# Optimization experiments

Hardware: AMD Instinct MI355X
Metric: run time of the kernel (lower is better)

## Reference

```python
import jax, jax.numpy as jnp
import numpy as np

D = 256  # input_dim
B = 2048

def setup_inputs() -> dict:
    key = jax.random.key(0)
    ks = jax.random.split(key, 6)
    x = jax.random.normal(ks[0], (B, D), dtype=jnp.float32)
    offsets = jax.random.normal(ks[1], (D,), dtype=jnp.float32)
    coeff0 = jax.random.normal(ks[2], (), dtype=jnp.float32)
    coeff1 = jax.random.normal(ks[3], (D,), dtype=jnp.float32)
    coeff2 = jax.random.normal(ks[4], (D, D), dtype=jnp.float32)
    coeff3 = jax.random.normal(ks[5], (D, D, D), dtype=jnp.float32)
    return {"x": x, "offsets": offsets, "coeff0": coeff0, "coeff1": coeff1,
            "coeff2": coeff2, "coeff3": coeff3}

def reference(x, offsets, coeff0, coeff1, coeff2, coeff3):
    # Truncated Taylor series around learned offsets: out[b] = c0 + sum_i <coeff_i, rel^{\otimes i}>[b]
    rel = x - offsets  # (B, D)
    out = coeff0  # scalar, broadcasts to (B,)
    for c in (coeff1, coeff2, coeff3):
        # contract one mode of the rank-i coefficient with rel at a time
        t = jnp.einsum('...d,bd->b...', c, rel)  # (B, D^{i-1})
        while t.ndim > 1:
            t = jnp.einsum('b...d,bd->b...', t, rel)
        out = out + t  # (B,)
    return out
```

## Files before the change

### kernel.cpp

```cpp
#include <hip/hip_runtime.h>
#include <hip/hip_bf16.h>

#define DD 256
#define BB 2048
#define BM 64
#define BN 64
#define NTILE 640
#define NSTAGE (BB / BN)

typedef __bf16 bf16x8 __attribute__((ext_vector_type(8)));
typedef float  f32x4  __attribute__((ext_vector_type(4)));

#define AS1 __attribute__((address_space(1)))
#define AS3 __attribute__((address_space(3)))

__device__ __forceinline__ unsigned short f2bf(float f) {
    unsigned int u = __float_as_uint(f);
    return (unsigned short)((u + 0x7FFFu + ((u >> 16) & 1u)) >> 16);
}
__device__ __forceinline__ float bf2f(unsigned short s) {
    return __uint_as_float(((unsigned int)s) << 16);
}
__device__ __forceinline__ void async_cp16(const void* g, void* l) {
    __builtin_amdgcn_global_load_lds((const AS1 unsigned int*)g,
                                     (AS3 unsigned int*)l, 16, 0, 0);
}

__global__ void prep_all(const float* __restrict__ x, const float* __restrict__ offsets,
                         const float* __restrict__ c0, const float* __restrict__ c1,
                         unsigned short* __restrict__ rel_bf16, float* __restrict__ out) {
    const int tid = threadIdx.x, wave = tid >> 6, lane = tid & 63;
    const float4 o4  = *(const float4*)(offsets + lane * 4);
    const float4 c14 = *(const float4*)(c1 + lane * 4);
#pragma unroll
    for (int i = 0; i < 2; ++i) {
        const int b = blockIdx.x * 8 + wave * 2 + i;
        const float4 x4 = *(const float4*)(x + (size_t)b * DD + lane * 4);
        float4 r;
        r.x = x4.x - o4.x; r.y = x4.y - o4.y; r.z = x4.z - o4.z; r.w = x4.w - o4.w;
        ushort4 rb;
        rb.x = f2bf(r.x); rb.y = f2bf(r.y); rb.z = f2bf(r.z); rb.w = f2bf(r.w);
        *(ushort4*)(rel_bf16 + (size_t)b * DD + lane * 4) = rb;
        float s = r.x * c14.x + r.y * c14.y + r.z * c14.z + r.w * c14.w;
        s += __shfl_xor(s, 1);  s += __shfl_xor(s, 2);  s += __shfl_xor(s, 4);
        s += __shfl_xor(s, 8);  s += __shfl_xor(s, 16); s += __shfl_xor(s, 32);
        if (lane == 0) out[b] = c0[0] + s;
    }
}

__global__ __launch_bounds__(256, 2) void taylor3(
    const float* __restrict__ c3, const float* __restrict__ c2,
    const unsigned short* __restrict__ rel_bf16, float* __restrict__ partial)
{
    __shared__ unsigned short Bs[2][BN * DD];
    __shared__ unsigned short relIbf[BB];
    __shared__ __align__(16) float B2row[BM];
    __shared__ float colsum[2][2][BN];

    const int bidx = blockIdx.x;
    int i_t, jt;
    if (bidx < 256)      { i_t = bidx >> 2;                jt = bidx & 3; }
    else if (bidx < 448) { const int u = bidx - 256; const int q = (u * 171) >> 9;
                           i_t = 64 + q;                   jt = 1 + (u - q * 3); }
    else if (bidx < 576) { const int u = bidx - 448;       i_t = 128 + (u >> 1); jt = 2 + (u & 1); }
    else                 { i_t = 192 + (bidx - 576);       jt = 3; }
    const int jbase = jt << 6;

    const int tid  = threadIdx.x;
    const int wave = tid >> 6;
    const int lane = tid & 63;
    const int wk = wave & 1, wn = wave >> 1;
    const int lrow = lane & 15, quad = lane >> 4;

#pragma unroll
    for (int k = 0; k < 8; ++k) {
        const int b = tid + k * 256;
        relIbf[b] = rel_bf16[(size_t)b * DD + i_t];
    }
    if (tid < BM) {
        const int j = jbase + tid;
        float v = 0.f;
        if (j > i_t)       v = c2[i_t * DD + j] + c2[j * DD + i_t];
        else if (j == i_t) v = c2[i_t * DD + j];
        B2row[tid] = v;
    }

    bf16x8 afr[4][4];
    {
#pragma unroll
        for (int mt = 0; mt < 4; ++mt) {
            const int j = jbase + mt * 16 + lrow;
            const float* p1 = c3 + ((size_t)i_t * DD + j) * DD + wk * 128 + quad * 8;
            const float* p2 = c3 + ((size_t)j * DD + i_t) * DD + wk * 128 + quad * 8;
#pragma unroll
            for (int ks = 0; ks < 4; ++ks) {
                float4 a0 = {0.f, 0.f, 0.f, 0.f}, a1 = {0.f, 0.f, 0.f, 0.f};
                if (j >= i_t) {
                    a0 = *(const float4*)(p1 + ks * 32);
                    a1 = *(const float4*)(p1 + ks * 32 + 4);
                    if (j > i_t) {
                        const float4 g0 = *(const float4*)(p2 + ks * 32);
                        const float4 g1 = *(const float4*)(p2 + ks * 32 + 4);
                        a0.x += g0.x; a0.y += g0.y; a0.z += g0.z; a0.w += g0.w;
                        a1.x += g1.x; a1.y += g1.y; a1.z += g1.z; a1.w += g1.w;
                    }
                }
                union { unsigned short u[8]; bf16x8 v; } cv;
                cv.u[0] = f2bf(a0.x); cv.u[1] = f2bf(a0.y);
                cv.u[2] = f2bf(a0.z); cv.u[3] = f2bf(a0.w);
                cv.u[4] = f2bf(a1.x); cv.u[5] = f2bf(a1.y);
                cv.u[6] = f2bf(a1.z); cv.u[7] = f2bf(a1.w);
                afr[ks][mt] = cv.v;
            }
        }
    }

    auto stage = [&](int nb, int buf) {
        const int b0 = nb * BN;
#pragma unroll
        for (int c = 0; c < 8; ++c) {
            const int r0 = c * 8 + wave * 2;
            const int row = r0 + (lane >> 5);
            const int g = (lane & 31) ^ (row & 7);
            const unsigned short* src = rel_bf16 + (size_t)(b0 + row) * DD + g * 8;
            async_cp16(src, &Bs[buf][r0 * DD]);
        }
    };

    auto body = [&](int nb, int cur) {
        const int b0 = nb * BN;
        __syncthreads();
        if (nb + 1 < NSTAGE) stage(nb + 1, cur ^ 1);

        if (nb > 0 && wave == 0) {
            const int pb0 = b0 - BN;
            const float v = colsum[cur ^ 1][0][lane] + colsum[cur ^ 1][1][lane];
            partial[(size_t)bidx * BB + pb0 + lane] = bf2f(relIbf[pb0 + lane]) * v;
        }

        f32x4 acc[4][2];
        __builtin_amdgcn_s_setprio(1);
        {
            const int glog = wk * 16 + quad;
            bf16x8 bfr[2];
#pragma unroll
            for (int nt = 0; nt < 2; ++nt) {
                const int col = wn * 32 + nt * 16 + lrow;
                const int g = glog ^ (col & 7);
                bfr[nt] = *(const bf16x8*)(&Bs[cur][col * DD + g * 8]);
            }
            const f32x4 z4 = (f32x4){0.f, 0.f, 0.f, 0.f};
#pragma unroll
            for (int mt = 0; mt < 4; ++mt)
#pragma unroll
                for (int nt = 0; nt < 2; ++nt)
                    acc[mt][nt] = __builtin_amdgcn_mfma_f32_16x16x32_bf16(
                        afr[0][mt], bfr[nt], z4, 0, 0, 0);
        }
#pragma unroll
        for (int ks = 1; ks < 4; ++ks) {
            const int glog = wk * 16 + ks * 4 + quad;
            bf16x8 bfr[2];
#pragma unroll
            for (int nt = 0; nt < 2; ++nt) {
                const int col = wn * 32 + nt * 16 + lrow;
                const int g = glog ^ (col & 7);
                bfr[nt] = *(const bf16x8*)(&Bs[cur][col * DD + g * 8]);
            }
#pragma unroll
            for (int mt = 0; mt < 4; ++mt)
#pragma unroll
                for (int nt = 0; nt < 2; ++nt)
                    acc[mt][nt] = __builtin_amdgcn_mfma_f32_16x16x32_bf16(
                        afr[ks][mt], bfr[nt], acc[mt][nt], 0, 0, 0);
        }
        __builtin_amdgcn_s_setprio(0);

        float sv[2];
#pragma unroll
        for (int nt = 0; nt < 2; ++nt) {
            const int col = wn * 32 + nt * 16 + lrow;
            float s0 = 0.f, s1 = 0.f;
#pragma unroll
            for (int mt = 0; mt < 4; ++mt) {
                const int e = mt * 16 + quad * 4;
                const int g = ((jbase + e) >> 3) ^ (col & 7);
                const ushort4 rj = *(const ushort4*)(&Bs[cur][col * DD + g * 8 + (e & 7)]);
                f32x4 a = acc[mt][nt];
                if (wk == 0) {
                    const float4 c2r = *(const float4*)(&B2row[e]);
                    a[0] += c2r.x; a[1] += c2r.y; a[2] += c2r.z; a[3] += c2r.w;
                }
                float& sa = (mt & 1) ? s1 : s0;
                sa = fmaf(a[0], bf2f(rj.x), sa);
                sa = fmaf(a[1], bf2f(rj.y), sa);
                sa = fmaf(a[2], bf2f(rj.z), sa);
                sa = fmaf(a[3], bf2f(rj.w), sa);
            }
            float s = s0 + s1;
            s += __shfl_xor(s, 16, 64);
            s += __shfl_xor(s, 32, 64);
            sv[nt] = s;
        }
        if (lane < 32)
            colsum[cur][wk][wn * 32 + lane] = (lane & 16) ? sv[1] : sv[0];
    };

    stage(0, 0);
    for (int nb = 0; nb < NSTAGE; nb += 2) {
        body(nb, 0);
        body(nb + 1, 1);
    }

    __syncthreads();
    if (wave == 0) {
        const int pb0 = BB - BN;
        const float v = colsum[1][0][lane] + colsum[1][1][lane];
        partial[(size_t)bidx * BB + pb0 + lane] = bf2f(relIbf[pb0 + lane]) * v;
    }
}

__global__ void reduce_partial(const float* __restrict__ partial, float* __restrict__ out) {
    __shared__ f32x4 red[256];
    const int t = threadIdx.x;
    const int g = blockIdx.x * 4 + (t & 3);
    const int slice = t >> 2;
    f32x4 s = (f32x4){0.f, 0.f, 0.f, 0.f};
    for (int r = slice * 10; r < slice * 10 + 10; ++r)
        s += *(const f32x4*)(partial + (size_t)r * BB + g * 4);
    red[t] = s; __syncthreads();
    if (t < 128) red[t] += red[t + 128]; __syncthreads();
    if (t < 64)  red[t] += red[t + 64];  __syncthreads();
    if (t < 32)  red[t] += red[t + 32];  __syncthreads();
    if (t < 16)  red[t] += red[t + 16];  __syncthreads();
    if (t < 8)   red[t] += red[t + 8];   __syncthreads();
    if (t < 4) {
        const f32x4 v = red[t] + red[t + 4];
        float4* op = (float4*)(out + (size_t)(blockIdx.x * 4 + t) * 4);
        float4 o = *op;
        o.x += v[0]; o.y += v[1]; o.z += v[2]; o.w += v[3];
        *op = o;
    }
}

extern "C" void kernel_launch(void* const* d_in, const int* in_sizes, int n_in,
                              void* d_out, int out_size, void* d_ws, size_t ws_size,
                              hipStream_t stream) {
    const float* x       = (const float*)d_in[0];
    const float* offsets = (const float*)d_in[1];
    const float* c0      = (const float*)d_in[2];
    const float* c1      = (const float*)d_in[3];
    const float* c2      = (const float*)d_in[4];
    const float* c3      = (const float*)d_in[5];
    float* out = (float*)d_out;

    char* ws = (char*)d_ws;
    unsigned short* rel_bf16 = (unsigned short*)ws;
    float* partial = (float*)(ws + (size_t)1 * 1024 * 1024);

    prep_all<<<BB / 8, 256, 0, stream>>>(x, offsets, c0, c1, rel_bf16, out);
    taylor3<<<NTILE, 256, 0, stream>>>(c3, c2, rel_bf16, partial);
    reduce_partial<<<128, 256, 0, stream>>>(partial, out);
}
```

Baseline: 220.9 us.

## Use one 1024-thread block per i slice with full j range, drop symmetry folding

The taylor3 kernel now launches one 1024-thread block per i index covering all 256 j columns, instead of 640 triangular 64-column tiles that folded c3[i,j,:] and c3[j,i,:] using symmetry. Each rel B-tile staged into LDS is now reused by 16 waves rather than 4, which cuts the redundant LDS staging of rel across tiles. In exchange the kernel does roughly twice the MFMA work and reads all of c3 without symmetric pairing, and the grid shrinks to 256 blocks, which may underfill the GPU. The partial reduction is adjusted to 256 rows, and the first stage load is issued before the coefficient loads to overlap them.

Result: slower. 242.8 us (+9.9%).

```diff
diff --git a/kernel.cpp b/kernel.cpp
--- a/kernel.cpp
+++ b/kernel.cpp
@@ -3,9 +3,9 @@
 
 #define DD 256
 #define BB 2048
-#define BM 64
+#define BM 256
 #define BN 64
-#define NTILE 640
+#define NTILE 256
 #define NSTAGE (BB / BN)
 
 typedef __bf16 bf16x8 __attribute__((ext_vector_type(8)));
@@ -48,78 +48,34 @@
     }
 }
 
-__global__ __launch_bounds__(256, 2) void taylor3(
+__global__ __launch_bounds__(1024, 4) void taylor3(
     const float* __restrict__ c3, const float* __restrict__ c2,
     const unsigned short* __restrict__ rel_bf16, float* __restrict__ partial)
 {
     __shared__ unsigned short Bs[2][BN * DD];
     __shared__ unsigned short relIbf[BB];
-    __shared__ __align__(16) float B2row[BM];
-    __shared__ float colsum[2][2][BN];
-
-    const int bidx = blockIdx.x;
-    int i_t, jt;
-    if (bidx < 256)      { i_t = bidx >> 2;                jt = bidx & 3; }
-    else if (bidx < 448) { const int u = bidx - 256; const int q = (u * 171) >> 9;
-                           i_t = 64 + q;                   jt = 1 + (u - q * 3); }
-    else if (bidx < 576) { const int u = bidx - 448;       i_t = 128 + (u >> 1); jt = 2 + (u & 1); }
-    else                 { i_t = 192 + (bidx - 576);       jt = 3; }
-    const int jbase = jt << 6;
-
+    __shared__ __align__(16) float c2row[DD];
+    __shared__ float colsum[2][8][BN];
+
+    const int i_t  = blockIdx.x;
     const int tid  = threadIdx.x;
     const int wave = tid >> 6;
     const int lane = tid & 63;
-    const int wk = wave & 1, wn = wave >> 1;
+    const int wm = wave & 3, wk = (wave >> 2) & 1, wn = wave >> 3;
     const int lrow = lane & 15, quad = lane >> 4;
 
 #pragma unroll
-    for (int k = 0; k < 8; ++k) {
-        const int b = tid + k * 256;
+    for (int k = 0; k < 2; ++k) {
+        const int b = tid + k * 1024;
         relIbf[b] = rel_bf16[(size_t)b * DD + i_t];
     }
-    if (tid < BM) {
-        const int j = jbase + tid;
-        float v = 0.f;
-        if (j > i_t)       v = c2[i_t * DD + j] + c2[j * DD + i_t];
-        else if (j == i_t) v = c2[i_t * DD + j];
-        B2row[tid] = v;
-    }
-
-    bf16x8 afr[4][4];
-    {
-#pragma unroll
-        for (int mt = 0; mt < 4; ++mt) {
-            const int j = jbase + mt * 16 + lrow;
-            const float* p1 = c3 + ((size_t)i_t * DD + j) * DD + wk * 128 + quad * 8;
-            const float* p2 = c3 + ((size_t)j * DD + i_t) * DD + wk * 128 + quad * 8;
-#pragma unroll
-            for (int ks = 0; ks < 4; ++ks) {
-                float4 a0 = {0.f, 0.f, 0.f, 0.f}, a1 = {0.f, 0.f, 0.f, 0.f};
-                if (j >= i_t) {
-                    a0 = *(const float4*)(p1 + ks * 32);
-                    a1 = *(const float4*)(p1 + ks * 32 + 4);
-                    if (j > i_t) {
-                        const float4 g0 = *(const float4*)(p2 + ks * 32);
-                        const float4 g1 = *(const float4*)(p2 + ks * 32 + 4);
-                        a0.x += g0.x; a0.y += g0.y; a0.z += g0.z; a0.w += g0.w;
-                        a1.x += g1.x; a1.y += g1.y; a1.z += g1.z; a1.w += g1.w;
-                    }
-                }
-                union { unsigned short u[8]; bf16x8 v; } cv;
-                cv.u[0] = f2bf(a0.x); cv.u[1] = f2bf(a0.y);
-                cv.u[2] = f2bf(a0.z); cv.u[3] = f2bf(a0.w);
-                cv.u[4] = f2bf(a1.x); cv.u[5] = f2bf(a1.y);
-                cv.u[6] = f2bf(a1.z); cv.u[7] = f2bf(a1.w);
-                afr[ks][mt] = cv.v;
-            }
-        }
-    }
+    if (tid < DD) c2row[tid] = c2[i_t * DD + tid];
 
     auto stage = [&](int nb, int buf) {
         const int b0 = nb * BN;
 #pragma unroll
-        for (int c = 0; c < 8; ++c) {
-            const int r0 = c * 8 + wave * 2;
+        for (int c = 0; c < 2; ++c) {
+            const int r0 = c * 32 + wave * 2;
             const int row = r0 + (lane >> 5);
             const int g = (lane & 31) ^ (row & 7);
             const unsigned short* src = rel_bf16 + (size_t)(b0 + row) * DD + g * 8;
@@ -127,6 +83,29 @@
         }
     };
 
+    stage(0, 0);
+
+    bf16x8 afr[4][4];
+    {
+        const float* abase = c3 + (size_t)i_t * DD * DD;
+#pragma unroll
+        for (int mt = 0; mt < 4; ++mt) {
+            const int j = wm * 64 + mt * 16 + lrow;
+            const float* p = abase + (size_t)j * DD + wk * 128 + quad * 8;
+#pragma unroll
+            for (int ks = 0; ks < 4; ++ks) {
+                const float4 f0 = *(const float4*)(p + ks * 32);
+                const float4 f1 = *(const float4*)(p + ks * 32 + 4);
+                union { unsigned short u[8]; bf16x8 v; } cv;
+                cv.u[0] = f2bf(f0.x); cv.u[1] = f2bf(f0.y);
+                cv.u[2] = f2bf(f0.z); cv.u[3] = f2bf(f0.w);
+                cv.u[4] = f2bf(f1.x); cv.u[5] = f2bf(f1.y);
+                cv.u[6] = f2bf(f1.z); cv.u[7] = f2bf(f1.w);
+                afr[ks][mt] = cv.v;
+            }
+        }
+    }
+
     auto body = [&](int nb, int cur) {
         const int b0 = nb * BN;
         __syncthreads();
@@ -134,8 +113,10 @@
 
         if (nb > 0 && wave == 0) {
             const int pb0 = b0 - BN;
-            const float v = colsum[cur ^ 1][0][lane] + colsum[cur ^ 1][1][lane];
-            partial[(size_t)bidx * BB + pb0 + lane] = bf2f(relIbf[pb0 + lane]) * v;
+            float v = colsum[cur ^ 1][0][lane];
+#pragma unroll
+            for (int w = 1; w < 8; ++w) v += colsum[cur ^ 1][w][lane];
+            partial[(size_t)i_t * BB + pb0 + lane] = bf2f(relIbf[pb0 + lane]) * v;
         }
 
         f32x4 acc[4][2];
@@ -183,12 +164,12 @@
             float s0 = 0.f, s1 = 0.f;
 #pragma unroll
             for (int mt = 0; mt < 4; ++mt) {
-                const int e = mt * 16 + quad * 4;
-                const int g = ((jbase + e) >> 3) ^ (col & 7);
+                const int e = wm * 64 + mt * 16 + quad * 4;
+                const int g = (e >> 3) ^ (col & 7);
                 const ushort4 rj = *(const ushort4*)(&Bs[cur][col * DD + g * 8 + (e & 7)]);
                 f32x4 a = acc[mt][nt];
                 if (wk == 0) {
-                    const float4 c2r = *(const float4*)(&B2row[e]);
+                    const float4 c2r = *(const float4*)(&c2row[e]);
                     a[0] += c2r.x; a[1] += c2r.y; a[2] += c2r.z; a[3] += c2r.w;
                 }
                 float& sa = (mt & 1) ? s1 : s0;
@@ -203,10 +184,9 @@
             sv[nt] = s;
         }
         if (lane < 32)
-            colsum[cur][wk][wn * 32 + lane] = (lane & 16) ? sv[1] : sv[0];
+            colsum[cur][wk * 4 + wm][wn * 32 + lane] = (lane & 16) ? sv[1] : sv[0];
     };
 
-    stage(0, 0);
     for (int nb = 0; nb < NSTAGE; nb += 2) {
         body(nb, 0);
         body(nb + 1, 1);
@@ -215,8 +195,10 @@
     __syncthreads();
     if (wave == 0) {
         const int pb0 = BB - BN;
-        const float v = colsum[1][0][lane] + colsum[1][1][lane];
-        partial[(size_t)bidx * BB + pb0 + lane] = bf2f(relIbf[pb0 + lane]) * v;
+        float v = colsum[1][0][lane];
+#pragma unroll
+        for (int w = 1; w < 8; ++w) v += colsum[1][w][lane];
+        partial[(size_t)i_t * BB + pb0 + lane] = bf2f(relIbf[pb0 + lane]) * v;
     }
 }
 
@@ -226,7 +208,7 @@
     const int g = blockIdx.x * 4 + (t & 3);
     const int slice = t >> 2;
     f32x4 s = (f32x4){0.f, 0.f, 0.f, 0.f};
-    for (int r = slice * 10; r < slice * 10 + 10; ++r)
+    for (int r = slice * 4; r < slice * 4 + 4; ++r)
         s += *(const f32x4*)(partial + (size_t)r * BB + g * 4);
     red[t] = s; __syncthreads();
     if (t < 128) red[t] += red[t + 128]; __syncthreads();
@@ -259,6 +241,6 @@
     float* partial = (float*)(ws + (size_t)1 * 1024 * 1024);
 
     prep_all<<<BB / 8, 256, 0, stream>>>(x, offsets, c0, c1, rel_bf16, out);
-    taylor3<<<NTILE, 256, 0, stream>>>(c3, c2, rel_bf16, partial);
+    taylor3<<<NTILE, 1024, 0, stream>>>(c3, c2, rel_bf16, partial);
     reduce_partial<<<128, 256, 0, stream>>>(partial, out);
 }
```
